# Kernel optimization log

Measured on AMD Instinct MI355X. Metric: run time of the kernel, lower is better.

## Reference

```python
import jax, jax.numpy as jnp
import numpy as np

N_NODES = 100000
N_EDGES = 1600000
HID = 64
EDGE_DIM = 32
N_LAYERS = 3
BN_EPS = 1e-5


def setup_inputs() -> dict:
    key = jax.random.key(0)
    ks = jax.random.split(key, 8)
    x = jax.random.normal(ks[0], (N_NODES, HID), dtype=jnp.float32)
    edge_index = jax.random.randint(ks[1], (2, N_EDGES), 0, N_NODES, dtype=jnp.int32)
    edge_attr = jax.random.normal(ks[2], (N_EDGES, EDGE_DIM), dtype=jnp.float32)
    s = 0.1  # small init scale for numerical stability
    We = jax.random.normal(ks[3], (N_LAYERS, EDGE_DIM, HID), dtype=jnp.float32) * s
    be = jnp.zeros((N_LAYERS, HID), jnp.float32)
    W1 = jax.random.normal(ks[4], (N_LAYERS, HID, HID), dtype=jnp.float32) * s
    b1 = jnp.zeros((N_LAYERS, HID), jnp.float32)
    W2 = jax.random.normal(ks[5], (N_LAYERS, HID, HID), dtype=jnp.float32) * s
    b2 = jnp.zeros((N_LAYERS, HID), jnp.float32)
    gamma = jnp.ones((N_LAYERS, HID), jnp.float32)
    beta = jnp.zeros((N_LAYERS, HID), jnp.float32)
    Wout = jax.random.normal(ks[6], (HID, HID), dtype=jnp.float32) * s
    bout = jnp.zeros((HID,), jnp.float32)
    return {"x": x, "edge_index": edge_index, "edge_attr": edge_attr,
            "We": We, "be": be, "W1": W1, "b1": b1, "W2": W2, "b2": b2,
            "gamma": gamma, "beta": beta, "Wout": Wout, "bout": bout}


def _forward(x, edge_index, edge_attr, We, be, W1, b1, W2, b2, gamma, beta, Wout, bout):
    src = edge_index[0]  # x_j (source of message)
    dst = edge_index[1]  # aggregation target
    n = x.shape[0]
    for i in range(N_LAYERS):
        # GINEConv: message = relu(x_j + lin_edge(edge_attr)); scatter-add to dst
        e = edge_attr @ We[i] + be[i]                      # [E, H]
        m = jax.nn.relu(x[src] + e)                        # [E, H] (dominant traffic)
        agg = jax.ops.segment_sum(m, dst, num_segments=n)  # [N, H]
        h = x + agg                                        # (1 + eps)*x, eps = 0
        # 2-layer MLP
        h = jax.nn.relu(h @ W1[i] + b1[i]) @ W2[i] + b2[i]
        # BatchNorm1d (training mode: batch statistics, biased variance)
        mean = jnp.mean(h, axis=0)
        var = jnp.var(h, axis=0)
        h = (h - mean) * jax.lax.rsqrt(var + BN_EPS) * gamma[i] + beta[i]
        x = jax.nn.relu(h)
    return x @ Wout + bout


def reference(x, edge_index, edge_attr, We, be, W1, b1, W2, b2, gamma, beta, Wout, bout):
    return _forward(x, edge_index, edge_attr, We, be, W1, b1, W2, b2, gamma, beta, Wout, bout)
```

## Files before the change

kernel.cpp:

```cpp
#include <hip/hip_runtime.h>

#define N_NODES 100000
#define N_EDGES 1600000
#define HID 64
#define EDIM 32
#define BN_EPS 1e-5f

#define SCAN_CHUNK 1024
#define NB_SCAN ((N_NODES + SCAN_CHUNK - 1) / SCAN_CHUNK)

#define G_NODES 16
#define CAP 320

__global__ __launch_bounds__(256) void hist_kernel(
    const int* __restrict__ dst, int* __restrict__ cnt)
{
    int i = (int)(blockIdx.x * blockDim.x + threadIdx.x);
    const int stride = (int)(gridDim.x * blockDim.x);
    for (; i < N_EDGES; i += stride) atomicAdd(&cnt[dst[i]], 1);
}

__global__ __launch_bounds__(256) void scan1_kernel(
    const int* __restrict__ cnt, int* __restrict__ bsum)
{
    __shared__ int s[256];
    const int b = (int)blockIdx.x, t = (int)threadIdx.x;
    const int base = b * SCAN_CHUNK + t * 4;
    int sum = 0;
#pragma unroll
    for (int k = 0; k < 4; ++k) {
        int idx = base + k;
        if (idx < N_NODES) sum += cnt[idx];
    }
    s[t] = sum;
    __syncthreads();
    for (int off = 128; off > 0; off >>= 1) {
        if (t < off) s[t] += s[t + off];
        __syncthreads();
    }
    if (t == 0) bsum[b] = s[0];
}

__global__ __launch_bounds__(128) void scan2_kernel(
    const int* __restrict__ bsum, int* __restrict__ bofs, int* __restrict__ row_ptr)
{
    __shared__ int s[128];
    const int t = (int)threadIdx.x;
    const int v = (t < NB_SCAN) ? bsum[t] : 0;
    s[t] = v;
    __syncthreads();
    for (int off = 1; off < 128; off <<= 1) {
        int add = (t >= off) ? s[t - off] : 0;
        __syncthreads();
        s[t] += add;
        __syncthreads();
    }
    if (t < NB_SCAN) bofs[t] = s[t] - v;
    if (t == NB_SCAN - 1) row_ptr[N_NODES] = s[t];
}

__global__ __launch_bounds__(256) void scan3_kernel(
    const int* __restrict__ cnt, const int* __restrict__ bofs,
    int* __restrict__ row_ptr, int* __restrict__ pos)
{
    __shared__ int s[256];
    const int b = (int)blockIdx.x, t = (int)threadIdx.x;
    const int base = b * SCAN_CHUNK + t * 4;
    int v[4];
    int sum = 0;
#pragma unroll
    for (int k = 0; k < 4; ++k) {
        int idx = base + k;
        v[k] = (idx < N_NODES) ? cnt[idx] : 0;
        sum += v[k];
    }
    s[t] = sum;
    __syncthreads();
    for (int off = 1; off < 256; off <<= 1) {
        int add = (t >= off) ? s[t - off] : 0;
        __syncthreads();
        s[t] += add;
        __syncthreads();
    }
    int run = s[t] - sum + bofs[b];
#pragma unroll
    for (int k = 0; k < 4; ++k) {
        int idx = base + k;
        if (idx < N_NODES) {
            row_ptr[idx] = run;
            pos[idx] = run;
            run += v[k];
        }
    }
}

__global__ __launch_bounds__(256) void scatter_kernel(
    const int* __restrict__ src, const int* __restrict__ dst,
    int* __restrict__ pos, int* __restrict__ perm_e, int* __restrict__ perm_src)
{
    int i = (int)(blockIdx.x * blockDim.x + threadIdx.x);
    const int stride = (int)(gridDim.x * blockDim.x);
    for (; i < N_EDGES; i += stride) {
        const int d = dst[i];
        const int p = atomicAdd(&pos[d], 1);
        perm_e[p] = i;
        perm_src[p] = src[i];
    }
}

__global__ __launch_bounds__(256) void gather_staged_kernel(
    const float* __restrict__ x, const float* __restrict__ eattr,
    const int* __restrict__ row_ptr, const int* __restrict__ perm_e,
    const int* __restrict__ perm_src,
    const float* __restrict__ We, const float* __restrict__ be,
    float* __restrict__ agg)
{
    __shared__ float s_attr[CAP * EDIM];
    __shared__ int   s_src[CAP];

    const int tid  = (int)threadIdx.x;
    const int lane = tid & 63;
    const int w    = tid >> 6;
    const int node_lo = (int)blockIdx.x * G_NODES;

    float wv[EDIM];
#pragma unroll
    for (int k = 0; k < EDIM; ++k) wv[k] = We[k * HID + lane];
    const float bias = be[lane];

    int rp[5];
#pragma unroll
    for (int i = 0; i < 5; ++i) {
        int n = node_lo + 4 * w + i;
        rp[i] = row_ptr[n < N_NODES ? n : N_NODES];
    }
    float acc[4] = {0.0f, 0.0f, 0.0f, 0.0f};

    const int e0 = row_ptr[node_lo < N_NODES ? node_lo : N_NODES];
    const int hi = node_lo + G_NODES;
    const int e1 = row_ptr[hi < N_NODES ? hi : N_NODES];

    for (int c0 = e0; c0 < e1; c0 += CAP) {
        const int cnt = (e1 - c0 < CAP) ? (e1 - c0) : CAP;
        __syncthreads();
        for (int i = tid; i < cnt * 8; i += 256) {
            const int row = i >> 3, part = i & 7;
            const int ep = perm_e[c0 + row];
            ((float4*)s_attr)[i] = ((const float4*)eattr)[(size_t)ep * 8 + part];
        }
        for (int i = tid; i < cnt; i += 256) s_src[i] = perm_src[c0 + i];
        __syncthreads();
        const int c1 = c0 + cnt;

#pragma unroll
        for (int q = 0; q < 4; ++q) {
            const int jb = (rp[q]     > c0) ? rp[q]     : c0;
            const int je = (rp[q + 1] < c1) ? rp[q + 1] : c1;
            float a = acc[q];
            int j = jb;
            if (j < je) {
                int s0 = s_src[j - c0];
                float xv = x[(size_t)s0 * HID + lane];
                while (j < je) {
                    const float4* p = (const float4*)(s_attr + (size_t)(j - c0) * EDIM);
                    const int jn = j + 1;
                    float xn = 0.0f;
                    if (jn < je) {
                        const int sn = s_src[jn - c0];
                        xn = x[(size_t)sn * HID + lane];
                    }
                    float e = bias;
#pragma unroll
                    for (int jj = 0; jj < 8; ++jj) {
                        const float4 qv = p[jj];
                        e = fmaf(qv.x, wv[4 * jj + 0], e);
                        e = fmaf(qv.y, wv[4 * jj + 1], e);
                        e = fmaf(qv.z, wv[4 * jj + 2], e);
                        e = fmaf(qv.w, wv[4 * jj + 3], e);
                    }
                    a += fmaxf(xv + e, 0.0f);
                    xv = xn;
                    j = jn;
                }
            }
            acc[q] = a;
        }
    }

#pragma unroll
    for (int q = 0; q < 4; ++q) {
        const int n = node_lo + 4 * w + q;
        if (n < N_NODES) agg[(size_t)n * HID + lane] = acc[q];
    }
}

__global__ __launch_bounds__(256) void mlp_kernel(
    const float* __restrict__ xin, const float* __restrict__ agg,
    const float* __restrict__ W1, const float* __restrict__ b1,
    const float* __restrict__ W2, const float* __restrict__ b2,
    float* __restrict__ uout)
{
    const int lane = threadIdx.x & 63;
    const int wid  = (int)((blockIdx.x * blockDim.x + threadIdx.x) >> 6);
    const int n    = wid * 64 + lane;
    const bool ok  = (n < N_NODES);
    const size_t base = (size_t)n * HID;

    float h[HID];
    if (ok) {
        const float4* px = (const float4*)(xin + base);
        const float4* pa = (const float4*)(agg + base);
#pragma unroll
        for (int j = 0; j < HID / 4; ++j) {
            float4 xv = px[j];
            float4 av = pa[j];
            h[4 * j + 0] = xv.x + av.x;
            h[4 * j + 1] = xv.y + av.y;
            h[4 * j + 2] = xv.z + av.z;
            h[4 * j + 3] = xv.w + av.w;
        }
    } else {
#pragma unroll
        for (int k = 0; k < HID; ++k) h[k] = 0.0f;
    }

    float u[HID];
#pragma unroll
    for (int f = 0; f < HID; ++f) u[f] = b2[f];

    for (int c = 0; c < 4; ++c) {
        float t[16];
#pragma unroll
        for (int j = 0; j < 16; ++j) t[j] = b1[c * 16 + j];
#pragma unroll
        for (int k = 0; k < HID; ++k) {
            const float hk = h[k];
#pragma unroll
            for (int j = 0; j < 16; ++j)
                t[j] = fmaf(hk, W1[k * HID + c * 16 + j], t[j]);
        }
#pragma unroll
        for (int j = 0; j < 16; ++j) t[j] = fmaxf(t[j], 0.0f);
#pragma unroll
        for (int j = 0; j < 16; ++j) {
            const float tj = t[j];
#pragma unroll
            for (int f = 0; f < HID; ++f)
                u[f] = fmaf(tj, W2[(c * 16 + j) * HID + f], u[f]);
        }
    }

    if (ok) {
        float4* po = (float4*)(uout + base);
#pragma unroll
        for (int j = 0; j < HID / 4; ++j)
            po[j] = make_float4(u[4 * j], u[4 * j + 1], u[4 * j + 2], u[4 * j + 3]);
    }
}

__global__ __launch_bounds__(256) void out_kernel(
    const float* __restrict__ xin, const float* __restrict__ Wo,
    const float* __restrict__ bo, float* __restrict__ out)
{
    const int lane = threadIdx.x & 63;
    const int wid  = (int)((blockIdx.x * blockDim.x + threadIdx.x) >> 6);
    const int n    = wid * 64 + lane;
    const bool ok  = (n < N_NODES);
    const size_t base = (size_t)n * HID;

    float h[HID];
    if (ok) {
        const float4* px = (const float4*)(xin + base);
#pragma unroll
        for (int j = 0; j < HID / 4; ++j) {
            float4 xv = px[j];
            h[4 * j + 0] = xv.x; h[4 * j + 1] = xv.y;
            h[4 * j + 2] = xv.z; h[4 * j + 3] = xv.w;
        }
    } else {
#pragma unroll
        for (int k = 0; k < HID; ++k) h[k] = 0.0f;
    }

    for (int c = 0; c < 4; ++c) {
        float t[16];
#pragma unroll
        for (int j = 0; j < 16; ++j) t[j] = bo[c * 16 + j];
#pragma unroll
        for (int k = 0; k < HID; ++k) {
            const float hk = h[k];
#pragma unroll
            for (int j = 0; j < 16; ++j)
                t[j] = fmaf(hk, Wo[k * HID + c * 16 + j], t[j]);
        }
        if (ok) {
            float4* po = (float4*)(out + base + c * 16);
#pragma unroll
            for (int j = 0; j < 4; ++j)
                po[j] = make_float4(t[4 * j], t[4 * j + 1], t[4 * j + 2], t[4 * j + 3]);
        }
    }
}

__global__ __launch_bounds__(256) void stats_kernel(
    const float* __restrict__ u, float* __restrict__ stats)
{
    __shared__ float ls[256];
    __shared__ float ls2[256];
    const int tid = (int)threadIdx.x;
    const int g   = (int)(blockIdx.x * 256 + tid);
    const int f   = g & 63;
    const int row = g >> 6;
    const int rstride = (int)((gridDim.x * 256) >> 6);

    float s = 0.0f, s2 = 0.0f;
    for (int n = row; n < N_NODES; n += rstride) {
        float v = u[(size_t)n * HID + f];
        s += v;
        s2 = fmaf(v, v, s2);
    }
    ls[tid] = s;
    ls2[tid] = s2;
    __syncthreads();
    if (tid < 64) {
        float a = ls[tid] + ls[tid + 64] + ls[tid + 128] + ls[tid + 192];
        float b = ls2[tid] + ls2[tid + 64] + ls2[tid + 128] + ls2[tid + 192];
        atomicAdd(&stats[tid], a);
        atomicAdd(&stats[64 + tid], b);
    }
}

__global__ __launch_bounds__(256) void bn_relu_kernel(
    const float* __restrict__ u, const float* __restrict__ stats,
    const float* __restrict__ gamma, const float* __restrict__ beta,
    float* __restrict__ xout)
{
    const int total4 = N_NODES * HID / 4;
    int i = (int)(blockIdx.x * blockDim.x + threadIdx.x);
    const int stride = (int)(gridDim.x * blockDim.x);
    const int fb = (i * 4) & 63;

    const float invN = 1.0f / (float)N_NODES;
    float sc[4], sh[4];
#pragma unroll
    for (int j = 0; j < 4; ++j) {
        float mean = stats[fb + j] * invN;
        float var  = stats[64 + fb + j] * invN - mean * mean;
        float s    = gamma[fb + j] * rsqrtf(var + BN_EPS);
        sc[j] = s;
        sh[j] = beta[fb + j] - mean * s;
    }
    for (; i < total4; i += stride) {
        float4 v = ((const float4*)u)[i];
        v.x = fmaxf(fmaf(v.x, sc[0], sh[0]), 0.0f);
        v.y = fmaxf(fmaf(v.y, sc[1], sh[1]), 0.0f);
        v.z = fmaxf(fmaf(v.z, sc[2], sh[2]), 0.0f);
        v.w = fmaxf(fmaf(v.w, sc[3], sh[3]), 0.0f);
        ((float4*)xout)[i] = v;
    }
}

extern "C" void kernel_launch(void* const* d_in, const int* in_sizes, int n_in,
                              void* d_out, int out_size, void* d_ws, size_t ws_size,
                              hipStream_t stream)
{
    const float* x0    = (const float*)d_in[0];
    const int*   eidx  = (const int*)d_in[1];
    const float* eattr = (const float*)d_in[2];
    const float* We    = (const float*)d_in[3];
    const float* be    = (const float*)d_in[4];
    const float* W1    = (const float*)d_in[5];
    const float* b1    = (const float*)d_in[6];
    const float* W2    = (const float*)d_in[7];
    const float* b2    = (const float*)d_in[8];
    const float* gamma = (const float*)d_in[9];
    const float* beta  = (const float*)d_in[10];
    const float* Wout  = (const float*)d_in[11];
    const float* bout  = (const float*)d_in[12];
    float* out = (float*)d_out;

    const int* src = eidx;
    const int* dst = eidx + N_EDGES;

    const size_t NH = (size_t)N_NODES * HID;

    float* A     = (float*)d_ws;
    float* AGG   = A + NH;
    float* stats = AGG + NH;
    int* cnt      = (int*)(stats + 128);
    int* bsum     = cnt + N_NODES;
    int* bofs     = bsum + 128;
    int* row_ptr  = bofs + 128;
    int* pos      = row_ptr + N_NODES + 1;
    int* perm_e   = pos + N_NODES;
    int* perm_src = perm_e + N_EDGES;
    float* B = out;

    hipMemsetAsync(cnt, 0, N_NODES * sizeof(int), stream);
    hist_kernel<<<1024, 256, 0, stream>>>(dst, cnt);
    scan1_kernel<<<NB_SCAN, 256, 0, stream>>>(cnt, bsum);
    scan2_kernel<<<1, 128, 0, stream>>>(bsum, bofs, row_ptr);
    scan3_kernel<<<NB_SCAN, 256, 0, stream>>>(cnt, bofs, row_ptr, pos);
    scatter_kernel<<<1024, 256, 0, stream>>>(src, dst, pos, perm_e, perm_src);

    const int mlp_blocks    = ((N_NODES + 63) / 64 + 3) / 4;
    const int gather_blocks = (N_NODES + G_NODES - 1) / G_NODES;

    const float* xin = x0;
    for (int i = 0; i < 3; ++i) {
        hipMemsetAsync(stats, 0, 128 * sizeof(float), stream);

        gather_staged_kernel<<<gather_blocks, 256, 0, stream>>>(
            xin, eattr, row_ptr, perm_e, perm_src,
            We + (size_t)i * EDIM * HID, be + (size_t)i * HID, AGG);

        mlp_kernel<<<mlp_blocks, 256, 0, stream>>>(
            xin, AGG,
            W1 + (size_t)i * HID * HID, b1 + (size_t)i * HID,
            W2 + (size_t)i * HID * HID, b2 + (size_t)i * HID, B);

        stats_kernel<<<256, 256, 0, stream>>>(B, stats);

        bn_relu_kernel<<<1024, 256, 0, stream>>>(
            B, stats, gamma + (size_t)i * HID, beta + (size_t)i * HID, A);

        xin = A;
    }

    out_kernel<<<mlp_blocks, 256, 0, stream>>>(A, Wout, bout, out);
}
```

Before: 1.747 ms.

## Compute edge projection with bf16 MFMA tiles staged in shared memory

Measured after the change: 2.469 ms. 41.3% more time.

```diff
diff --git a/kernel.cpp b/kernel.cpp
--- a/kernel.cpp
+++ b/kernel.cpp
@@ -10,7 +10,17 @@
 #define NB_SCAN ((N_NODES + SCAN_CHUNK - 1) / SCAN_CHUNK)
 
 #define G_NODES 16
-#define CAP 320
+#define CAP 128
+#define ES 68
+
+typedef __attribute__((ext_vector_type(8))) short short8;
+typedef __attribute__((ext_vector_type(4))) float f32x4;
+
+__device__ __forceinline__ short bf16_rne(float f) {
+    union { float f; unsigned u; } v; v.f = f;
+    unsigned r = v.u + 0x7FFFu + ((v.u >> 16) & 1u);
+    return (short)(r >> 16);
+}
 
 __global__ __launch_bounds__(256) void hist_kernel(
     const int* __restrict__ dst, int* __restrict__ cnt)
@@ -108,25 +118,32 @@
     }
 }
 
-__global__ __launch_bounds__(256) void gather_staged_kernel(
+__global__ __launch_bounds__(256) void gather_mfma_kernel(
     const float* __restrict__ x, const float* __restrict__ eattr,
     const int* __restrict__ row_ptr, const int* __restrict__ perm_e,
     const int* __restrict__ perm_src,
     const float* __restrict__ We, const float* __restrict__ be,
     float* __restrict__ agg)
 {
-    __shared__ float s_attr[CAP * EDIM];
-    __shared__ int   s_src[CAP];
+    __shared__ float s_e[CAP * ES];
 
     const int tid  = (int)threadIdx.x;
     const int lane = tid & 63;
     const int w    = tid >> 6;
     const int node_lo = (int)blockIdx.x * G_NODES;
 
-    float wv[EDIM];
-#pragma unroll
-    for (int k = 0; k < EDIM; ++k) wv[k] = We[k * HID + lane];
-    const float bias = be[lane];
+    const int col = lane & 15;
+    const int kg  = lane >> 4;
+
+    short8 bfrag[4];
+    float  be_n[4];
+#pragma unroll
+    for (int nt = 0; nt < 4; ++nt) {
+#pragma unroll
+        for (int j = 0; j < 8; ++j)
+            bfrag[nt][j] = bf16_rne(We[(kg * 8 + j) * HID + nt * 16 + col]);
+        be_n[nt] = be[nt * 16 + col];
+    }
 
     int rp[5];
 #pragma unroll
@@ -141,14 +158,33 @@
     const int e1 = row_ptr[hi < N_NODES ? hi : N_NODES];
 
     for (int c0 = e0; c0 < e1; c0 += CAP) {
-        const int cnt = (e1 - c0 < CAP) ? (e1 - c0) : CAP;
-        __syncthreads();
-        for (int i = tid; i < cnt * 8; i += 256) {
-            const int row = i >> 3, part = i & 7;
-            const int ep = perm_e[c0 + row];
-            ((float4*)s_attr)[i] = ((const float4*)eattr)[(size_t)ep * 8 + part];
-        }
-        for (int i = tid; i < cnt; i += 256) s_src[i] = perm_src[c0 + i];
+        const int cnt    = (e1 - c0 < CAP) ? (e1 - c0) : CAP;
+        const int ntiles = (cnt + 15) >> 4;
+        __syncthreads();
+
+        for (int t = w; t < ntiles; t += 4) {
+            int gi = c0 + t * 16 + col;
+            if (gi > e1 - 1) gi = e1 - 1;
+            const int er = perm_e[gi];
+            const float4* pa = (const float4*)(eattr + (size_t)er * EDIM + kg * 8);
+            const float4 a0 = pa[0];
+            const float4 a1 = pa[1];
+            short8 afrag;
+            afrag[0] = bf16_rne(a0.x); afrag[1] = bf16_rne(a0.y);
+            afrag[2] = bf16_rne(a0.z); afrag[3] = bf16_rne(a0.w);
+            afrag[4] = bf16_rne(a1.x); afrag[5] = bf16_rne(a1.y);
+            afrag[6] = bf16_rne(a1.z); afrag[7] = bf16_rne(a1.w);
+
+            const int erow = t * 16 + kg * 4;
+#pragma unroll
+            for (int nt = 0; nt < 4; ++nt) {
+                f32x4 c = {0.0f, 0.0f, 0.0f, 0.0f};
+                c = __builtin_amdgcn_mfma_f32_16x16x32_bf16(afrag, bfrag[nt], c, 0, 0, 0);
+#pragma unroll
+                for (int r = 0; r < 4; ++r)
+                    s_e[(erow + r) * ES + nt * 16 + col] = c[r] + be_n[nt];
+            }
+        }
         __syncthreads();
         const int c1 = c0 + cnt;
 
@@ -157,30 +193,18 @@
             const int jb = (rp[q]     > c0) ? rp[q]     : c0;
             const int je = (rp[q + 1] < c1) ? rp[q + 1] : c1;
             float a = acc[q];
-            int j = jb;
-            if (j < je) {
-                int s0 = s_src[j - c0];
+            if (jb < je) {
+                int s0 = perm_src[jb];
                 float xv = x[(size_t)s0 * HID + lane];
-                while (j < je) {
-                    const float4* p = (const float4*)(s_attr + (size_t)(j - c0) * EDIM);
-                    const int jn = j + 1;
+                for (int j = jb; j < je; ++j) {
+                    const float ev = s_e[(j - c0) * ES + lane];
                     float xn = 0.0f;
-                    if (jn < je) {
-                        const int sn = s_src[jn - c0];
+                    if (j + 1 < je) {
+                        const int sn = perm_src[j + 1];
                         xn = x[(size_t)sn * HID + lane];
                     }
-                    float e = bias;
-#pragma unroll
-                    for (int jj = 0; jj < 8; ++jj) {
-                        const float4 qv = p[jj];
-                        e = fmaf(qv.x, wv[4 * jj + 0], e);
-                        e = fmaf(qv.y, wv[4 * jj + 1], e);
-                        e = fmaf(qv.z, wv[4 * jj + 2], e);
-                        e = fmaf(qv.w, wv[4 * jj + 3], e);
-                    }
-                    a += fmaxf(xv + e, 0.0f);
+                    a += fmaxf(xv + ev, 0.0f);
                     xv = xn;
-                    j = jn;
                 }
             }
             acc[q] = a;
@@ -410,7 +434,7 @@
     for (int i = 0; i < 3; ++i) {
         hipMemsetAsync(stats, 0, 128 * sizeof(float), stream);
 
-        gather_staged_kernel<<<gather_blocks, 256, 0, stream>>>(
+        gather_mfma_kernel<<<gather_blocks, 256, 0, stream>>>(
             xin, eattr, row_ptr, perm_e, perm_src,
             We + (size_t)i * EDIM * HID, be + (size_t)i * HID, AGG);
 
```
